# Performance work log

Measured on AMD Instinct MI355X. Metric: run time of the kernel, lower is better.

Reference implementation:

```python
import jax, jax.numpy as jnp
import numpy as np

N_NODES = 98304
N_GRAPHS = 2048
NODES_PER_GRAPH = 48
N_EDGES = 393216
NODE_IN = 128
EMB = 64
HID = 256
N_LAYERS = 6
ATTN_DIM = 256
N_HEADS = 4
HEAD_DIM = ATTN_DIM // N_HEADS
OUT_DIM = 1024


def setup_inputs() -> dict:
    key = jax.random.key(0)
    ks = iter(jax.random.split(key, 40))

    def nrm(shape, fan_in):
        return (jax.random.normal(next(ks), shape, dtype=jnp.float32)
                / np.float32(np.sqrt(fan_in)))

    x = jax.random.normal(next(ks), (N_NODES, NODE_IN), dtype=jnp.float32)
    edge_index = jax.random.randint(next(ks), (2, N_EDGES), 0, N_NODES, dtype=jnp.int32)
    batch = (jnp.arange(N_NODES, dtype=jnp.int32) // NODES_PER_GRAPH)

    inp = {
        "x": x,
        "edge_index": edge_index,
        "batch": batch,
        "W_embed": nrm((NODE_IN, EMB), NODE_IN),
        "b_embed": jnp.zeros((EMB,), jnp.float32),
        "W1": nrm((N_LAYERS, EMB, HID), EMB),
        "b1": jnp.zeros((N_LAYERS, HID), jnp.float32),
        "W2": nrm((N_LAYERS, HID, 2 * HID), HID),
        "b2": jnp.zeros((N_LAYERS, 2 * HID), jnp.float32),
        "W3": nrm((N_LAYERS, 2 * HID, EMB), 2 * HID),
        "b3": jnp.zeros((N_LAYERS, EMB), jnp.float32),
        "Wp": nrm((EMB, ATTN_DIM), EMB),
        "bp": jnp.zeros((ATTN_DIM,), jnp.float32),
        "q": jax.random.normal(next(ks), (1, ATTN_DIM), dtype=jnp.float32),
        "W_in": nrm((ATTN_DIM, 3 * ATTN_DIM), ATTN_DIM),
        "b_in": jnp.zeros((3 * ATTN_DIM,), jnp.float32),
        "W_out": nrm((ATTN_DIM, ATTN_DIM), ATTN_DIM),
        "b_out": jnp.zeros((ATTN_DIM,), jnp.float32),
        "Wh1": nrm((ATTN_DIM, HID), ATTN_DIM),
        "bh1": jnp.zeros((HID,), jnp.float32),
        "ln_g": jnp.ones((HID,), jnp.float32),
        "ln_b": jnp.zeros((HID,), jnp.float32),
        "Wh2": nrm((HID, OUT_DIM), HID),
        "bh2": jnp.zeros((OUT_DIM,), jnp.float32),
    }
    return inp


def _forward(x, edge_index, batch, W_embed, b_embed, W1, b1, W2, b2, W3, b3,
             Wp, bp, q, W_in, b_in, W_out, b_out, Wh1, bh1, ln_g, ln_b, Wh2, bh2):
    row = edge_index[0]  # only row is used, matching the torch module

    # node embed
    h = x @ W_embed + b_embed  # [N, 64]

    # 6 GNN layers: gather h[row] -> 3-layer MLP -> scatter_add back to row
    for l in range(N_LAYERS):
        m = jax.nn.relu(h[row] @ W1[l] + b1[l])          # [E, 256]
        m = jax.nn.relu(m @ W2[l] + b2[l])               # [E, 512]
        dh = m @ W3[l] + b3[l]                           # [E, 64]
        h = h + jax.ops.segment_sum(dh, row, num_segments=N_NODES)

    # attention pooling per graph (single learned query, 4 heads)
    hp = h @ Wp + bp                                     # [N, 256]
    Wq, Wk, Wv = W_in[:, :ATTN_DIM], W_in[:, ATTN_DIM:2 * ATTN_DIM], W_in[:, 2 * ATTN_DIM:]
    bq, bk, bv = b_in[:ATTN_DIM], b_in[ATTN_DIM:2 * ATTN_DIM], b_in[2 * ATTN_DIM:]

    qh = ((q @ Wq + bq).reshape(N_HEADS, HEAD_DIM)
          / jnp.asarray(np.sqrt(HEAD_DIM), jnp.float32))  # [H, D]
    k = (hp @ Wk + bk).reshape(N_NODES, N_HEADS, HEAD_DIM)
    v = (hp @ Wv + bv).reshape(N_NODES, N_HEADS, HEAD_DIM)

    scores = jnp.einsum('nhd,hd->nh', k, qh)             # [N, H]
    smax = jax.ops.segment_max(scores, batch, num_segments=N_GRAPHS)  # [B, H]
    e = jnp.exp(scores - smax[batch])
    denom = jax.ops.segment_sum(e, batch, num_segments=N_GRAPHS)      # [B, H]
    w = e / denom[batch]                                  # [N, H]
    pooled = jax.ops.segment_sum(w[:, :, None] * v, batch, num_segments=N_GRAPHS)  # [B, H, D]
    attn = pooled.reshape(N_GRAPHS, ATTN_DIM) @ W_out + b_out  # [B, 256]

    # projection head: ReLU -> Linear -> ReLU -> LayerNorm -> Linear
    t = jax.nn.relu(attn) @ Wh1 + bh1
    t = jax.nn.relu(t)
    mu = jnp.mean(t, axis=-1, keepdims=True)
    var = jnp.mean((t - mu) ** 2, axis=-1, keepdims=True)
    t = (t - mu) * jax.lax.rsqrt(var + 1e-5) * ln_g + ln_b
    return t @ Wh2 + bh2                                  # [B, 1024]


def reference(x, edge_index, batch, W_embed, b_embed, W1, b1, W2, b2, W3, b3,
              Wp, bp, q, W_in, b_in, W_out, b_out, Wh1, bh1, ln_g, ln_b, Wh2, bh2):
    return _forward(x, edge_index, batch, W_embed, b_embed, W1, b1, W2, b2, W3, b3,
                    Wp, bp, q, W_in, b_in, W_out, b_out, Wh1, bh1, ln_g, ln_b, Wh2, bh2)
```

## Files before the change

kernel.cpp:

```cpp
#include <hip/hip_runtime.h>
#include <hip/hip_bf16.h>

#define N_NODES 98304
#define N_GRAPHS 2048
#define N_EDGES 393216
#define EMB 64
#define HID 256
#define N_LAYERS_ 6

typedef __attribute__((ext_vector_type(8))) short short8v;
typedef __attribute__((ext_vector_type(4))) float f32x4;
#define MFMA16(a, b, c) __builtin_amdgcn_mfma_f32_16x16x32_bf16(a, b, c, 0, 0, 0)

__device__ __forceinline__ unsigned short f2bf(float x) {
    unsigned int u = __float_as_uint(x);
    u = (u + 0x7fffu + ((u >> 16) & 1u)) >> 16;
    return (unsigned short)u;
}
__device__ __forceinline__ float bf2f(unsigned short h) {
    return __uint_as_float(((unsigned int)h) << 16);
}
__device__ __forceinline__ unsigned int cvtpk(float a, float b) {
    unsigned int r;
    asm("v_cvt_pk_bf16_f32 %0, %1, %2" : "=v"(r) : "v"(a), "v"(b));
    return r;
}
__device__ __forceinline__ int swz(int row, int col, int rowc) {
    return (row * rowc + col) ^ ((row & 7) << 3);
}

__global__ __launch_bounds__(256) void zero_cnt_kernel(int* __restrict__ cnt) {
    int i = blockIdx.x * 256 + threadIdx.x;
    if (i < N_NODES) cnt[i] = 0;
}
__global__ __launch_bounds__(256) void hist_kernel(const int* __restrict__ row,
                                                   int* __restrict__ cnt) {
    int i = blockIdx.x * 256 + threadIdx.x;
    if (i < N_EDGES) atomicAdd(&cnt[row[i]], 1);
}

__global__ __launch_bounds__(64) void prep_frag_kernel(
    const float* __restrict__ W, unsigned short* __restrict__ oh,
    unsigned short* __restrict__ ol, int K, int N)
{
    const int NF = N >> 4, KS = K >> 5;
    const int fpl = NF * KS;
    const int layer = blockIdx.x / fpl;
    const int fid = blockIdx.x % fpl;
    const int nf = fid / KS, ks = fid % KS;
    const int lane = threadIdx.x;
    const float* Wl = W + (size_t)layer * K * N;
    const int n = nf * 16 + (lane & 15);
    const int kb = ks * 32 + (lane >> 4) * 8;
    short8v vh, vl;
    #pragma unroll
    for (int j = 0; j < 8; j++) {
        float wv = Wl[(size_t)(kb + j) * N + n];
        unsigned short hi = f2bf(wv);
        vh[j] = (short)hi;
        vl[j] = (short)f2bf(wv - bf2f(hi));
    }
    size_t o = (size_t)layer * K * N + ((size_t)(nf * KS + ks) * 64 + lane) * 8;
    *reinterpret_cast<short8v*>(oh + o) = vh;
    *reinterpret_cast<short8v*>(ol + o) = vl;
}

__global__ __launch_bounds__(256) void gbuild_kernel(
    const float* __restrict__ Wp, const float* __restrict__ bp,
    const float* __restrict__ W_in, const float* __restrict__ b_in,
    float* __restrict__ Gm, float* __restrict__ Gd)
{
    const int idx = blockIdx.x * 256 + threadIdx.x;
    const int q = idx >> 8, p = idx & 255;
    float s = 0.f;
    if ((q >> 6) == (p >> 6)) {
        const float* wr = Wp + (q & 63) * 256;
        for (int j = 0; j < 256; j++) s += wr[j] * W_in[j * 768 + 512 + p];
    }
    Gm[q * 256 + p] = s;
    if (blockIdx.x == 0) {
        const int pp = threadIdx.x;
        float dsum = b_in[512 + pp];
        for (int j = 0; j < 256; j++) dsum += bp[j] * W_in[j * 768 + 512 + pp];
        Gd[pp] = dsum;
    }
}

__global__ __launch_bounds__(256) void embed_mfma_kernel(
    const float* __restrict__ x,
    const unsigned short* __restrict__ Weh, const unsigned short* __restrict__ Wel,
    const float* __restrict__ b, float* __restrict__ h)
{
    __shared__ __attribute__((aligned(16))) unsigned short xh[32 * 128];
    __shared__ __attribute__((aligned(16))) unsigned short xl[32 * 128];
    const int tid = threadIdx.x;
    const int lane = tid & 63, w = tid >> 6;
    const int lm = lane & 15, lq = lane >> 4;
    const int base = blockIdx.x * 32;
    {
        int row = tid >> 3, c0 = (tid & 7) * 16;
        const float4* p = reinterpret_cast<const float4*>(x + (size_t)(base + row) * 128 + c0);
        #pragma unroll
        for (int g = 0; g < 4; g++) {
            float4 u = p[g];
            unsigned int p01 = cvtpk(u.x, u.y);
            unsigned int p23 = cvtpk(u.z, u.w);
            float h0 = __uint_as_float(p01 << 16), h1 = __uint_as_float(p01 & 0xffff0000u);
            float h2 = __uint_as_float(p23 << 16), h3 = __uint_as_float(p23 & 0xffff0000u);
            unsigned int q01 = cvtpk(u.x - h0, u.y - h1);
            unsigned int q23 = cvtpk(u.z - h2, u.w - h3);
            int idx = swz(row, c0 + g * 4, 128);
            *reinterpret_cast<uint2*>(&xh[idx]) = make_uint2(p01, p23);
            *reinterpret_cast<uint2*>(&xl[idx]) = make_uint2(q01, q23);
        }
    }
    __syncthreads();
    f32x4 acc0, acc1;
    {
        float bv = b[w * 16 + lm];
        acc0 = f32x4{bv, bv, bv, bv};
        acc1 = acc0;
    }
    #pragma unroll
    for (int ks = 0; ks < 4; ks++) {
        short8v a0h = *reinterpret_cast<const short8v*>(&xh[swz(lm, ks * 32 + lq * 8, 128)]);
        short8v a0l = *reinterpret_cast<const short8v*>(&xl[swz(lm, ks * 32 + lq * 8, 128)]);
        short8v a1h = *reinterpret_cast<const short8v*>(&xh[swz(16 + lm, ks * 32 + lq * 8, 128)]);
        short8v a1l = *reinterpret_cast<const short8v*>(&xl[swz(16 + lm, ks * 32 + lq * 8, 128)]);
        size_t bi = ((size_t)(w * 4 + ks) * 64 + lane) * 8;
        short8v bh = *reinterpret_cast<const short8v*>(Weh + bi);
        short8v bl = *reinterpret_cast<const short8v*>(Wel + bi);
        acc0 = MFMA16(a0h, bh, acc0); acc0 = MFMA16(a0l, bh, acc0); acc0 = MFMA16(a0h, bl, acc0);
        acc1 = MFMA16(a1h, bh, acc1); acc1 = MFMA16(a1l, bh, acc1); acc1 = MFMA16(a1h, bl, acc1);
    }
    #pragma unroll
    for (int r = 0; r < 4; r++) {
        h[(size_t)(base + lq * 4 + r) * 64 + w * 16 + lm] = acc0[r];
        h[(size_t)(base + 16 + lq * 4 + r) * 64 + w * 16 + lm] = acc1[r];
    }
}

__device__ __forceinline__ void store_quad(
    unsigned short* __restrict__ oh, unsigned short* __restrict__ ol,
    float v0, float v1, float v2, float v3,
    int row0, int col, int rowc)
{
    unsigned int p01 = cvtpk(v0, v1);
    unsigned int p23 = cvtpk(v2, v3);
    float h0 = __uint_as_float(p01 << 16), h1 = __uint_as_float(p01 & 0xffff0000u);
    float h2 = __uint_as_float(p23 << 16), h3 = __uint_as_float(p23 & 0xffff0000u);
    unsigned int q01 = cvtpk(v0 - h0, v1 - h1);
    unsigned int q23 = cvtpk(v2 - h2, v3 - h3);
    oh[swz(row0 + 0, col, rowc)] = (unsigned short)p01;
    oh[swz(row0 + 1, col, rowc)] = (unsigned short)(p01 >> 16);
    oh[swz(row0 + 2, col, rowc)] = (unsigned short)p23;
    oh[swz(row0 + 3, col, rowc)] = (unsigned short)(p23 >> 16);
    ol[swz(row0 + 0, col, rowc)] = (unsigned short)q01;
    ol[swz(row0 + 1, col, rowc)] = (unsigned short)(q01 >> 16);
    ol[swz(row0 + 2, col, rowc)] = (unsigned short)q23;
    ol[swz(row0 + 3, col, rowc)] = (unsigned short)(q23 >> 16);
}

__global__ __launch_bounds__(512, 6) void layer_mfma_kernel(
    float* __restrict__ h, const int* __restrict__ cnt,
    const unsigned short* __restrict__ W1h, const unsigned short* __restrict__ W1l,
    const float* __restrict__ b1,
    const unsigned short* __restrict__ W2h, const unsigned short* __restrict__ W2l,
    const float* __restrict__ b2,
    const unsigned short* __restrict__ W3h, const unsigned short* __restrict__ W3l,
    const float* __restrict__ b3)
{
    __shared__ __attribute__((aligned(16))) unsigned short R0[4096];
    __shared__ __attribute__((aligned(16))) unsigned short m1h_[8192];
    __shared__ __attribute__((aligned(16))) unsigned short m1l_[8192];
    __shared__ __attribute__((aligned(16))) unsigned short m2l_[4096];
    unsigned short* hsh = R0;
    unsigned short* hsl = R0 + 2048;
    unsigned short* m2h_ = R0;
    const int tid = threadIdx.x;
    const int lane = tid & 63, w = tid >> 6;
    const int lm = lane & 15, lq = lane >> 4;
    const int base = blockIdx.x * 32;

    {
        int row = tid >> 4, c0 = (tid & 15) * 4;
        const float4 u = *reinterpret_cast<const float4*>(h + (size_t)(base + row) * 64 + c0);
        unsigned int p01 = cvtpk(u.x, u.y);
        unsigned int p23 = cvtpk(u.z, u.w);
        float h0 = __uint_as_float(p01 << 16), h1 = __uint_as_float(p01 & 0xffff0000u);
        float h2 = __uint_as_float(p23 << 16), h3 = __uint_as_float(p23 & 0xffff0000u);
        unsigned int q01 = cvtpk(u.x - h0, u.y - h1);
        unsigned int q23 = cvtpk(u.z - h2, u.w - h3);
        int idx = swz(row, c0, 64);
        *reinterpret_cast<uint2*>(&hsh[idx]) = make_uint2(p01, p23);
        *reinterpret_cast<uint2*>(&hsl[idx]) = make_uint2(q01, q23);
    }
    __syncthreads();

    {
        f32x4 acc[2][2];
        #pragma unroll
        for (int f = 0; f < 2; f++) {
            float bv = b1[(2 * w + f) * 16 + lm];
            acc[f][0] = f32x4{bv, bv, bv, bv};
            acc[f][1] = acc[f][0];
        }
        #pragma unroll
        for (int ks = 0; ks < 2; ks++) {
            short8v ah0 = *reinterpret_cast<const short8v*>(&hsh[swz(lm, ks * 32 + lq * 8, 64)]);
            short8v al0 = *reinterpret_cast<const short8v*>(&hsl[swz(lm, ks * 32 + lq * 8, 64)]);
            short8v ah1 = *reinterpret_cast<const short8v*>(&hsh[swz(16 + lm, ks * 32 + lq * 8, 64)]);
            short8v al1 = *reinterpret_cast<const short8v*>(&hsl[swz(16 + lm, ks * 32 + lq * 8, 64)]);
            #pragma unroll
            for (int f = 0; f < 2; f++) {
                size_t bi = ((size_t)((2 * w + f) * 2 + ks) * 64 + lane) * 8;
                short8v bh = *reinterpret_cast<const short8v*>(W1h + bi);
                short8v bl = *reinterpret_cast<const short8v*>(W1l + bi);
                acc[f][0] = MFMA16(ah0, bh, acc[f][0]);
                acc[f][0] = MFMA16(al0, bh, acc[f][0]);
                acc[f][0] = MFMA16(ah0, bl, acc[f][0]);
                acc[f][1] = MFMA16(ah1, bh, acc[f][1]);
                acc[f][1] = MFMA16(al1, bh, acc[f][1]);
                acc[f][1] = MFMA16(ah1, bl, acc[f][1]);
            }
        }
        #pragma unroll
        for (int f = 0; f < 2; f++)
            #pragma unroll
            for (int m = 0; m < 2; m++)
                store_quad(m1h_, m1l_,
                           fmaxf(acc[f][m][0], 0.f), fmaxf(acc[f][m][1], 0.f),
                           fmaxf(acc[f][m][2], 0.f), fmaxf(acc[f][m][3], 0.f),
                           m * 16 + lq * 4, (2 * w + f) * 16 + lm, 256);
    }
    __syncthreads();

    const int nfc = w & 3, kq = w >> 2;
    f32x4 dacc[2];
    if (kq == 0) {
        float bv = b3[nfc * 16 + lm];
        dacc[0] = f32x4{bv, bv, bv, bv};
    } else {
        dacc[0] = f32x4{0.f, 0.f, 0.f, 0.f};
    }
    dacc[1] = dacc[0];

    #pragma unroll
    for (int c = 0; c < 4; ++c) {
        {
            const int nfg = c * 8 + w;
            f32x4 acc[2];
            {
                float bv = b2[nfg * 16 + lm];
                acc[0] = f32x4{bv, bv, bv, bv};
                acc[1] = acc[0];
            }
            #pragma unroll
            for (int ks = 0; ks < 8; ks++) {
                short8v ah0 = *reinterpret_cast<const short8v*>(&m1h_[swz(lm, ks * 32 + lq * 8, 256)]);
                short8v al0 = *reinterpret_cast<const short8v*>(&m1l_[swz(lm, ks * 32 + lq * 8, 256)]);
                short8v ah1 = *reinterpret_cast<const short8v*>(&m1h_[swz(16 + lm, ks * 32 + lq * 8, 256)]);
                short8v al1 = *reinterpret_cast<const short8v*>(&m1l_[swz(16 + lm, ks * 32 + lq * 8, 256)]);
                size_t bi = ((size_t)(nfg * 8 + ks) * 64 + lane) * 8;
                short8v bh = *reinterpret_cast<const short8v*>(W2h + bi);
                short8v bl = *reinterpret_cast<const short8v*>(W2l + bi);
                acc[0] = MFMA16(ah0, bh, acc[0]);
                acc[0] = MFMA16(al0, bh, acc[0]);
                acc[0] = MFMA16(ah0, bl, acc[0]);
                acc[1] = MFMA16(ah1, bh, acc[1]);
                acc[1] = MFMA16(al1, bh, acc[1]);
                acc[1] = MFMA16(ah1, bl, acc[1]);
            }
            #pragma unroll
            for (int m = 0; m < 2; m++)
                store_quad(m2h_, m2l_,
                           fmaxf(acc[m][0], 0.f), fmaxf(acc[m][1], 0.f),
                           fmaxf(acc[m][2], 0.f), fmaxf(acc[m][3], 0.f),
                           m * 16 + lq * 4, w * 16 + lm, 128);
        }
        __syncthreads();
        {
            #pragma unroll
            for (int kl = 0; kl < 2; kl++) {
                int ksl = kq * 2 + kl;
                short8v ah0 = *reinterpret_cast<const short8v*>(&m2h_[swz(lm, ksl * 32 + lq * 8, 128)]);
                short8v al0 = *reinterpret_cast<const short8v*>(&m2l_[swz(lm, ksl * 32 + lq * 8, 128)]);
                short8v ah1 = *reinterpret_cast<const short8v*>(&m2h_[swz(16 + lm, ksl * 32 + lq * 8, 128)]);
                short8v al1 = *reinterpret_cast<const short8v*>(&m2l_[swz(16 + lm, ksl * 32 + lq * 8, 128)]);
                int ksg = c * 4 + ksl;
                size_t bi = ((size_t)(nfc * 16 + ksg) * 64 + lane) * 8;
                short8v bh = *reinterpret_cast<const short8v*>(W3h + bi);
                short8v bl = *reinterpret_cast<const short8v*>(W3l + bi);
                dacc[0] = MFMA16(ah0, bh, dacc[0]);
                dacc[0] = MFMA16(al0, bh, dacc[0]);
                dacc[0] = MFMA16(ah0, bl, dacc[0]);
                dacc[1] = MFMA16(ah1, bh, dacc[1]);
                dacc[1] = MFMA16(al1, bh, dacc[1]);
                dacc[1] = MFMA16(ah1, bl, dacc[1]);
            }
        }
        __syncthreads();
    }

    float* scr = reinterpret_cast<float*>(m1h_);
    if (kq == 1) {
        #pragma unroll
        for (int m = 0; m < 2; m++)
            #pragma unroll
            for (int r = 0; r < 4; r++)
                scr[(m * 16 + lq * 4 + r) * 64 + nfc * 16 + lm] = dacc[m][r];
    }
    __syncthreads();
    if (kq == 0) {
        #pragma unroll
        for (int m = 0; m < 2; m++)
            #pragma unroll
            for (int r = 0; r < 4; r++) {
                int rr = base + m * 16 + lq * 4 + r;
                float dv = dacc[m][r] + scr[(m * 16 + lq * 4 + r) * 64 + nfc * 16 + lm];
                size_t gi = (size_t)rr * 64 + nfc * 16 + lm;
                h[gi] = h[gi] + (float)cnt[rr] * dv;
            }
    }
}

__global__ __launch_bounds__(256) void prec_kernel(
    const float* __restrict__ q, const float* __restrict__ W_in,
    const float* __restrict__ b_in, const float* __restrict__ Wp,
    const float* __restrict__ bp, float* __restrict__ prec)
{
    __shared__ float qh_s[256];
    __shared__ float u_s[4 * 256];
    const int tid = threadIdx.x;
    {
        float acc = b_in[tid];
        for (int j = 0; j < 256; j++) acc += q[j] * W_in[j * 768 + tid];
        qh_s[tid] = acc * 0.125f;
    }
    __syncthreads();
    {
        #pragma unroll
        for (int hd = 0; hd < 4; hd++) {
            float a = 0.f;
            for (int d = 0; d < 64; d++)
                a += W_in[tid * 768 + 256 + hd * 64 + d] * qh_s[hd * 64 + d];
            u_s[hd * 256 + tid] = a;
        }
    }
    __syncthreads();
    {
        int hd = tid >> 6, i = tid & 63;
        float a = 0.f;
        for (int j = 0; j < 256; j++) a += Wp[i * 256 + j] * u_s[hd * 256 + j];
        prec[hd * 64 + i] = a;
    }
    if (tid < 4) {
        float a = 0.f;
        for (int j = 0; j < 256; j++) a += bp[j] * u_s[tid * 256 + j];
        for (int d = 0; d < 64; d++) a += b_in[256 + tid * 64 + d] * qh_s[tid * 64 + d];
        prec[256 + tid] = a;
    }
}

__global__ __launch_bounds__(64) void attnpool_kernel(
    const float* __restrict__ h, const float* __restrict__ prec,
    float* __restrict__ hw)
{
    __shared__ float hs[48 * 65];
    __shared__ float ss[4 * 64];
    __shared__ float ds_[4];
    __shared__ float wl[48 * 4];
    const int lane = threadIdx.x;
    const int g = blockIdx.x;
    #pragma unroll
    for (int hd = 0; hd < 4; hd++) ss[hd * 64 + lane] = prec[hd * 64 + lane];
    if (lane < 4) ds_[lane] = prec[256 + lane];
    for (int r = 0; r < 48; r++)
        hs[r * 65 + lane] = h[((size_t)g * 48 + r) * 64 + lane];
    __syncthreads();
    float sc[4] = {0.f, 0.f, 0.f, 0.f};
    if (lane < 48) {
        #pragma unroll
        for (int hd = 0; hd < 4; hd++) sc[hd] = ds_[hd];
        for (int c = 0; c < 64; c++) {
            float a = hs[lane * 65 + c];
            #pragma unroll
            for (int hd = 0; hd < 4; hd++) sc[hd] += a * ss[hd * 64 + c];
        }
    }
    #pragma unroll
    for (int hd = 0; hd < 4; hd++) {
        float v = (lane < 48) ? sc[hd] : -3.0e38f;
        #pragma unroll
        for (int m = 32; m >= 1; m >>= 1) v = fmaxf(v, __shfl_xor(v, m, 64));
        float e = (lane < 48) ? __expf(sc[hd] - v) : 0.f;
        float s = e;
        #pragma unroll
        for (int m = 32; m >= 1; m >>= 1) s += __shfl_xor(s, m, 64);
        if (lane < 48) wl[lane * 4 + hd] = e / s;
    }
    __syncthreads();
    float acc[4] = {0.f, 0.f, 0.f, 0.f};
    for (int n = 0; n < 48; n++) {
        float hv = hs[n * 65 + lane];
        #pragma unroll
        for (int hd = 0; hd < 4; hd++) acc[hd] += wl[n * 4 + hd] * hv;
    }
    #pragma unroll
    for (int hd = 0; hd < 4; hd++) hw[(size_t)g * 256 + hd * 64 + lane] = acc[hd];
}

__device__ __forceinline__ void tail_stage(
    const unsigned short* __restrict__ inh, const unsigned short* __restrict__ inl,
    const unsigned short* __restrict__ wh, const unsigned short* __restrict__ wl,
    const float* __restrict__ bias, const bool do_relu,
    unsigned short* __restrict__ oth, unsigned short* __restrict__ otl,
    float* __restrict__ tf32,
    const int w, const int lane, const int lm, const int lq)
{
    f32x4 acc[2][2];
    #pragma unroll
    for (int f = 0; f < 2; f++) {
        float bv = bias[(2 * w + f) * 16 + lm];
        acc[f][0] = f32x4{bv, bv, bv, bv};
        acc[f][1] = acc[f][0];
    }
    #pragma unroll
    for (int ks = 0; ks < 8; ks++) {
        short8v ah0 = *reinterpret_cast<const short8v*>(&inh[swz(lm, ks * 32 + lq * 8, 256)]);
        short8v al0 = *reinterpret_cast<const short8v*>(&inl[swz(lm, ks * 32 + lq * 8, 256)]);
        short8v ah1 = *reinterpret_cast<const short8v*>(&inh[swz(16 + lm, ks * 32 + lq * 8, 256)]);
        short8v al1 = *reinterpret_cast<const short8v*>(&inl[swz(16 + lm, ks * 32 + lq * 8, 256)]);
        #pragma unroll
        for (int f = 0; f < 2; f++) {
            size_t bi = ((size_t)((2 * w + f) * 8 + ks) * 64 + lane) * 8;
            short8v bh = *reinterpret_cast<const short8v*>(wh + bi);
            short8v bl = *reinterpret_cast<const short8v*>(wl + bi);
            acc[f][0] = MFMA16(ah0, bh, acc[f][0]);
            acc[f][0] = MFMA16(al0, bh, acc[f][0]);
            acc[f][0] = MFMA16(ah0, bl, acc[f][0]);
            acc[f][1] = MFMA16(ah1, bh, acc[f][1]);
            acc[f][1] = MFMA16(al1, bh, acc[f][1]);
            acc[f][1] = MFMA16(ah1, bl, acc[f][1]);
        }
    }
    #pragma unroll
    for (int f = 0; f < 2; f++)
        #pragma unroll
        for (int m = 0; m < 2; m++) {
            if (tf32) {
                #pragma unroll
                for (int r = 0; r < 4; r++) {
                    float v = acc[f][m][r];
                    if (do_relu) v = fmaxf(v, 0.f);
                    tf32[(m * 16 + lq * 4 + r) * 256 + (2 * w + f) * 16 + lm] = v;
                }
            } else {
                float v0 = acc[f][m][0], v1 = acc[f][m][1], v2 = acc[f][m][2], v3 = acc[f][m][3];
                if (do_relu) {
                    v0 = fmaxf(v0, 0.f); v1 = fmaxf(v1, 0.f);
                    v2 = fmaxf(v2, 0.f); v3 = fmaxf(v3, 0.f);
                }
                store_quad(oth, otl, v0, v1, v2, v3,
                           m * 16 + lq * 4, (2 * w + f) * 16 + lm, 256);
            }
        }
}

__global__ __launch_bounds__(512, 4) void tail_mfma_kernel(
    const float* __restrict__ hw,
    const unsigned short* __restrict__ Gh, const unsigned short* __restrict__ Gl,
    const float* __restrict__ Gd,
    const unsigned short* __restrict__ Woh, const unsigned short* __restrict__ Wol,
    const float* __restrict__ b_out,
    const unsigned short* __restrict__ Wh1h, const unsigned short* __restrict__ Wh1l,
    const float* __restrict__ bh1,
    const float* __restrict__ ln_g, const float* __restrict__ ln_b,
    const unsigned short* __restrict__ Wh2h, const unsigned short* __restrict__ Wh2l,
    const float* __restrict__ bh2,
    float* __restrict__ out)
{
    __shared__ __attribute__((aligned(16))) unsigned short L[32768];
    unsigned short* Ah = L;
    unsigned short* Al = L + 8192;
    unsigned short* Bh = L + 16384;
    unsigned short* Bl = L + 24576;
    float* tf = reinterpret_cast<float*>(L + 16384);
    const int tid = threadIdx.x;
    const int lane = tid & 63, w = tid >> 6;
    const int lm = lane & 15, lq = lane >> 4;
    const int g0 = blockIdx.x * 32;

    {
        const float4* hp = reinterpret_cast<const float4*>(hw + (size_t)g0 * 256);
        #pragma unroll
        for (int i = 0; i < 4; i++) {
            int e = tid + 512 * i;
            int row = e >> 6, c0 = (e & 63) * 4;
            float4 u = hp[e];
            unsigned int p01 = cvtpk(u.x, u.y);
            unsigned int p23 = cvtpk(u.z, u.w);
            float h0 = __uint_as_float(p01 << 16), h1 = __uint_as_float(p01 & 0xffff0000u);
            float h2 = __uint_as_float(p23 << 16), h3 = __uint_as_float(p23 & 0xffff0000u);
            unsigned int q01 = cvtpk(u.x - h0, u.y - h1);
            unsigned int q23 = cvtpk(u.z - h2, u.w - h3);
            int idx = swz(row, c0, 256);
            *reinterpret_cast<uint2*>(&Ah[idx]) = make_uint2(p01, p23);
            *reinterpret_cast<uint2*>(&Al[idx]) = make_uint2(q01, q23);
        }
    }
    __syncthreads();
    tail_stage(Ah, Al, Gh, Gl, Gd, false, Bh, Bl, nullptr, w, lane, lm, lq);
    __syncthreads();
    tail_stage(Bh, Bl, Woh, Wol, b_out, true, Ah, Al, nullptr, w, lane, lm, lq);
    __syncthreads();
    tail_stage(Ah, Al, Wh1h, Wh1l, bh1, true, nullptr, nullptr, tf, w, lane, lm, lq);
    __syncthreads();
    {
        const int row = tid >> 4, l16 = tid & 15;
        float s = 0.f;
        #pragma unroll
        for (int k = 0; k < 16; k++) s += tf[row * 256 + l16 + 16 * k];
        #pragma unroll
        for (int m = 1; m < 16; m <<= 1) s += __shfl_xor(s, m, 16);
        float mu = s * (1.f / 256.f);
        float v = 0.f;
        #pragma unroll
        for (int k = 0; k < 16; k++) {
            float d = tf[row * 256 + l16 + 16 * k] - mu;
            v += d * d;
        }
        #pragma unroll
        for (int m = 1; m < 16; m <<= 1) v += __shfl_xor(v, m, 16);
        float rs = rsqrtf(v * (1.f / 256.f) + 1e-5f);
        #pragma unroll
        for (int k = 0; k < 16; k++) {
            int col = l16 + 16 * k;
            float val = (tf[row * 256 + col] - mu) * rs * ln_g[col] + ln_b[col];
            unsigned short hi = f2bf(val);
            int idx = swz(row, col, 256);
            Ah[idx] = hi;
            Al[idx] = f2bf(val - bf2f(hi));
        }
    }
    __syncthreads();
    {
        f32x4 acc[8][2];
        #pragma unroll
        for (int f = 0; f < 8; f++) {
            float bv = bh2[(8 * w + f) * 16 + lm];
            acc[f][0] = f32x4{bv, bv, bv, bv};
            acc[f][1] = acc[f][0];
        }
        #pragma unroll
        for (int ks = 0; ks < 8; ks++) {
            short8v ah0 = *reinterpret_cast<const short8v*>(&Ah[swz(lm, ks * 32 + lq * 8, 256)]);
            short8v al0 = *reinterpret_cast<const short8v*>(&Al[swz(lm, ks * 32 + lq * 8, 256)]);
            short8v ah1 = *reinterpret_cast<const short8v*>(&Ah[swz(16 + lm, ks * 32 + lq * 8, 256)]);
            short8v al1 = *reinterpret_cast<const short8v*>(&Al[swz(16 + lm, ks * 32 + lq * 8, 256)]);
            #pragma unroll
            for (int f = 0; f < 8; f++) {
                size_t bi = ((size_t)((8 * w + f) * 8 + ks) * 64 + lane) * 8;
                short8v bh = *reinterpret_cast<const short8v*>(Wh2h + bi);
                short8v bl = *reinterpret_cast<const short8v*>(Wh2l + bi);
                acc[f][0] = MFMA16(ah0, bh, acc[f][0]);
                acc[f][0] = MFMA16(al0, bh, acc[f][0]);
                acc[f][0] = MFMA16(ah0, bl, acc[f][0]);
                acc[f][1] = MFMA16(ah1, bh, acc[f][1]);
                acc[f][1] = MFMA16(al1, bh, acc[f][1]);
                acc[f][1] = MFMA16(ah1, bl, acc[f][1]);
            }
        }
        #pragma unroll
        for (int f = 0; f < 8; f++)
            #pragma unroll
            for (int m = 0; m < 2; m++)
                #pragma unroll
                for (int r = 0; r < 4; r++)
                    out[(size_t)(g0 + m * 16 + lq * 4 + r) * 1024 + (8 * w + f) * 16 + lm]
                        = acc[f][m][r];
    }
}

extern "C" void kernel_launch(void* const* d_in, const int* in_sizes, int n_in,
                              void* d_out, int out_size, void* d_ws, size_t ws_size,
                              hipStream_t stream) {
    const float* x       = (const float*)d_in[0];
    const int*   edge    = (const int*)d_in[1];
    const float* W_embed = (const float*)d_in[3];
    const float* b_embed = (const float*)d_in[4];
    const float* W1 = (const float*)d_in[5];
    const float* b1 = (const float*)d_in[6];
    const float* W2 = (const float*)d_in[7];
    const float* b2 = (const float*)d_in[8];
    const float* W3 = (const float*)d_in[9];
    const float* b3 = (const float*)d_in[10];
    const float* Wp = (const float*)d_in[11];
    const float* bp = (const float*)d_in[12];
    const float* q  = (const float*)d_in[13];
    const float* W_in  = (const float*)d_in[14];
    const float* b_in  = (const float*)d_in[15];
    const float* W_out = (const float*)d_in[16];
    const float* b_out = (const float*)d_in[17];
    const float* Wh1 = (const float*)d_in[18];
    const float* bh1 = (const float*)d_in[19];
    const float* ln_g = (const float*)d_in[20];
    const float* ln_b = (const float*)d_in[21];
    const float* Wh2 = (const float*)d_in[22];
    const float* bh2 = (const float*)d_in[23];
    float* out = (float*)d_out;

    char* ws = (char*)d_ws;
    int*   cnt  = (int*)(ws + 0);
    float* h    = (float*)(ws + 393216);
    float* hw   = (float*)(ws + 25559040);
    float* prec = (float*)(ws + 27656192);
    unsigned short* W1h = (unsigned short*)(ws + 27657232);
    unsigned short* W1l = (unsigned short*)(ws + 27853840);
    unsigned short* W2h = (unsigned short*)(ws + 28050448);
    unsigned short* W2l = (unsigned short*)(ws + 29623312);
    unsigned short* W3h = (unsigned short*)(ws + 31196176);
    unsigned short* W3l = (unsigned short*)(ws + 31589392);
    unsigned short* Weh = (unsigned short*)(ws + 31982608);
    unsigned short* Wel = (unsigned short*)(ws + 31998992);
    float* Gm  = (float*)(ws + 32015376);
    float* Gd  = (float*)(ws + 32277520);
    unsigned short* Gfh  = (unsigned short*)(ws + 32278544);
    unsigned short* Gfl  = (unsigned short*)(ws + 32409616);
    unsigned short* Wofh = (unsigned short*)(ws + 32540688);
    unsigned short* Wofl = (unsigned short*)(ws + 32671760);
    unsigned short* Wh1fh= (unsigned short*)(ws + 32802832);
    unsigned short* Wh1fl= (unsigned short*)(ws + 32933904);
    unsigned short* Wh2fh= (unsigned short*)(ws + 33064976);
    unsigned short* Wh2fl= (unsigned short*)(ws + 33589264);

    zero_cnt_kernel<<<N_NODES / 256, 256, 0, stream>>>(cnt);
    hist_kernel<<<N_EDGES / 256, 256, 0, stream>>>(edge, cnt);

    prep_frag_kernel<<<1 * (64 / 16) * (128 / 32), 64, 0, stream>>>(W_embed, Weh, Wel, 128, 64);
    prep_frag_kernel<<<6 * (256 / 16) * (64 / 32), 64, 0, stream>>>(W1, W1h, W1l, 64, 256);
    prep_frag_kernel<<<6 * (512 / 16) * (256 / 32), 64, 0, stream>>>(W2, W2h, W2l, 256, 512);
    prep_frag_kernel<<<6 * (64 / 16) * (512 / 32), 64, 0, stream>>>(W3, W3h, W3l, 512, 64);

    gbuild_kernel<<<256, 256, 0, stream>>>(Wp, bp, W_in, b_in, Gm, Gd);
    prep_frag_kernel<<<(256 / 16) * (256 / 32), 64, 0, stream>>>(Gm, Gfh, Gfl, 256, 256);
    prep_frag_kernel<<<(256 / 16) * (256 / 32), 64, 0, stream>>>(W_out, Wofh, Wofl, 256, 256);
    prep_frag_kernel<<<(256 / 16) * (256 / 32), 64, 0, stream>>>(Wh1, Wh1fh, Wh1fl, 256, 256);
    prep_frag_kernel<<<(1024 / 16) * (256 / 32), 64, 0, stream>>>(Wh2, Wh2fh, Wh2fl, 256, 1024);

    embed_mfma_kernel<<<N_NODES / 32, 256, 0, stream>>>(x, Weh, Wel, b_embed, h);
    for (int l = 0; l < N_LAYERS_; l++) {
        layer_mfma_kernel<<<N_NODES / 32, 512, 0, stream>>>(
            h, cnt,
            W1h + (size_t)l * EMB * HID,     W1l + (size_t)l * EMB * HID,     b1 + (size_t)l * HID,
            W2h + (size_t)l * HID * 2 * HID, W2l + (size_t)l * HID * 2 * HID, b2 + (size_t)l * 2 * HID,
            W3h + (size_t)l * 2 * HID * EMB, W3l + (size_t)l * 2 * HID * EMB, b3 + (size_t)l * EMB);
    }
    prec_kernel<<<1, 256, 0, stream>>>(q, W_in, b_in, Wp, bp, prec);
    attnpool_kernel<<<N_GRAPHS, 64, 0, stream>>>(h, prec, hw);
    tail_mfma_kernel<<<N_GRAPHS / 32, 512, 0, stream>>>(
        hw, Gfh, Gfl, Gd, Wofh, Wofl, b_out, Wh1fh, Wh1fl, bh1,
        ln_g, ln_b, Wh2fh, Wh2fl, bh2, out);
}
```

Measured before the change: 877.5 us.

## Switch GNN layer kernel to 32x32x16 MFMA with wider chunks and new LDS plan

Rewrites the per-layer MLP kernel to use 32x32x16 bf16 MFMA tiles instead of 16x16x32. Weights are pre-fragmented in the matching 32-wide layout, W2 is processed in two 256-column chunks instead of four 128-column chunks, and the final reduction goes through a 4-way LDS scratch with a vectorised float4 update of h. The goal is fewer B-fragment loads per MFMA and fewer barriers and chunk iterations. In exchange, LDS grows to 64 KB per block, occupancy is lowered to 4 waves per SIMD, and an extra barrier is added inside each chunk.

```diff
diff --git a/kernel.cpp b/kernel.cpp
--- a/kernel.cpp
+++ b/kernel.cpp
@@ -10,7 +10,9 @@
 
 typedef __attribute__((ext_vector_type(8))) short short8v;
 typedef __attribute__((ext_vector_type(4))) float f32x4;
+typedef __attribute__((ext_vector_type(16))) float f32x16;
 #define MFMA16(a, b, c) __builtin_amdgcn_mfma_f32_16x16x32_bf16(a, b, c, 0, 0, 0)
+#define MFMA32(a, b, c) __builtin_amdgcn_mfma_f32_32x32x16_bf16(a, b, c, 0, 0, 0)
 
 __device__ __forceinline__ unsigned short f2bf(float x) {
     unsigned int u = __float_as_uint(x);
@@ -26,7 +28,7 @@
     return r;
 }
 __device__ __forceinline__ int swz(int row, int col, int rowc) {
-    return (row * rowc + col) ^ ((row & 7) << 3);
+    return (row * rowc + col) ^ ((row & ((rowc >> 3) - 1)) << 3);
 }
 
 __global__ __launch_bounds__(256) void zero_cnt_kernel(int* __restrict__ cnt) {
@@ -52,6 +54,32 @@
     const float* Wl = W + (size_t)layer * K * N;
     const int n = nf * 16 + (lane & 15);
     const int kb = ks * 32 + (lane >> 4) * 8;
+    short8v vh, vl;
+    #pragma unroll
+    for (int j = 0; j < 8; j++) {
+        float wv = Wl[(size_t)(kb + j) * N + n];
+        unsigned short hi = f2bf(wv);
+        vh[j] = (short)hi;
+        vl[j] = (short)f2bf(wv - bf2f(hi));
+    }
+    size_t o = (size_t)layer * K * N + ((size_t)(nf * KS + ks) * 64 + lane) * 8;
+    *reinterpret_cast<short8v*>(oh + o) = vh;
+    *reinterpret_cast<short8v*>(ol + o) = vl;
+}
+
+__global__ __launch_bounds__(64) void prep_frag32_kernel(
+    const float* __restrict__ W, unsigned short* __restrict__ oh,
+    unsigned short* __restrict__ ol, int K, int N)
+{
+    const int NF = N >> 5, KS = K >> 4;
+    const int fpl = NF * KS;
+    const int layer = blockIdx.x / fpl;
+    const int fid = blockIdx.x % fpl;
+    const int nf = fid / KS, ks = fid % KS;
+    const int lane = threadIdx.x;
+    const float* Wl = W + (size_t)layer * K * N;
+    const int n = nf * 32 + (lane & 31);
+    const int kb = ks * 16 + (lane >> 5) * 8;
     short8v vh, vl;
     #pragma unroll
     for (int j = 0; j < 8; j++) {
@@ -161,7 +189,7 @@
     ol[swz(row0 + 3, col, rowc)] = (unsigned short)(q23 >> 16);
 }
 
-__global__ __launch_bounds__(512, 6) void layer_mfma_kernel(
+__global__ __launch_bounds__(512, 4) void layer_mfma_kernel(
     float* __restrict__ h, const int* __restrict__ cnt,
     const unsigned short* __restrict__ W1h, const unsigned short* __restrict__ W1l,
     const float* __restrict__ b1,
@@ -170,16 +198,19 @@
     const unsigned short* __restrict__ W3h, const unsigned short* __restrict__ W3l,
     const float* __restrict__ b3)
 {
-    __shared__ __attribute__((aligned(16))) unsigned short R0[4096];
-    __shared__ __attribute__((aligned(16))) unsigned short m1h_[8192];
-    __shared__ __attribute__((aligned(16))) unsigned short m1l_[8192];
-    __shared__ __attribute__((aligned(16))) unsigned short m2l_[4096];
-    unsigned short* hsh = R0;
-    unsigned short* hsl = R0 + 2048;
-    unsigned short* m2h_ = R0;
+    __shared__ __attribute__((aligned(16))) unsigned short m1_[16384];
+    __shared__ __attribute__((aligned(16))) unsigned short m2_[16384];
+    unsigned short* m1h_ = m1_;
+    unsigned short* m1l_ = m1_ + 8192;
+    unsigned short* m2h_ = m2_;
+    unsigned short* m2l_ = m2_ + 8192;
+    unsigned short* hsh = m2_;
+    unsigned short* hsl = m2_ + 2048;
+    float* scr = reinterpret_cast<float*>(m1_);
+
     const int tid = threadIdx.x;
     const int lane = tid & 63, w = tid >> 6;
-    const int lm = lane & 15, lq = lane >> 4;
+    const int lr = lane & 31, lh = lane >> 5;
     const int base = blockIdx.x * 32;
 
     {
@@ -198,129 +229,118 @@
     __syncthreads();
 
     {
-        f32x4 acc[2][2];
-        #pragma unroll
-        for (int f = 0; f < 2; f++) {
-            float bv = b1[(2 * w + f) * 16 + lm];
-            acc[f][0] = f32x4{bv, bv, bv, bv};
-            acc[f][1] = acc[f][0];
-        }
-        #pragma unroll
-        for (int ks = 0; ks < 2; ks++) {
-            short8v ah0 = *reinterpret_cast<const short8v*>(&hsh[swz(lm, ks * 32 + lq * 8, 64)]);
-            short8v al0 = *reinterpret_cast<const short8v*>(&hsl[swz(lm, ks * 32 + lq * 8, 64)]);
-            short8v ah1 = *reinterpret_cast<const short8v*>(&hsh[swz(16 + lm, ks * 32 + lq * 8, 64)]);
-            short8v al1 = *reinterpret_cast<const short8v*>(&hsl[swz(16 + lm, ks * 32 + lq * 8, 64)]);
+        f32x16 a0, a1;
+        float bv = b1[w * 32 + lr];
+        #pragma unroll
+        for (int i = 0; i < 16; i++) { a0[i] = bv; a1[i] = 0.f; }
+        #pragma unroll
+        for (int ks = 0; ks < 4; ks++) {
+            short8v ah = *reinterpret_cast<const short8v*>(&hsh[swz(lr, ks * 16 + lh * 8, 64)]);
+            short8v al = *reinterpret_cast<const short8v*>(&hsl[swz(lr, ks * 16 + lh * 8, 64)]);
+            size_t bi = ((size_t)(w * 4 + ks) * 64 + lane) * 8;
+            short8v bh = *reinterpret_cast<const short8v*>(W1h + bi);
+            short8v bl = *reinterpret_cast<const short8v*>(W1l + bi);
+            if (ks & 1) {
+                a1 = MFMA32(ah, bh, a1); a1 = MFMA32(al, bh, a1); a1 = MFMA32(ah, bl, a1);
+            } else {
+                a0 = MFMA32(ah, bh, a0); a0 = MFMA32(al, bh, a0); a0 = MFMA32(ah, bl, a0);
+            }
+        }
+        #pragma unroll
+        for (int q = 0; q < 4; q++)
+            store_quad(m1h_, m1l_,
+                fmaxf(a0[4 * q + 0] + a1[4 * q + 0], 0.f),
+                fmaxf(a0[4 * q + 1] + a1[4 * q + 1], 0.f),
+                fmaxf(a0[4 * q + 2] + a1[4 * q + 2], 0.f),
+                fmaxf(a0[4 * q + 3] + a1[4 * q + 3], 0.f),
+                8 * q + 4 * lh, w * 32 + lr, 256);
+    }
+    __syncthreads();
+
+    const int nfc = w & 1, kq = w >> 1;
+    f32x16 d0, d1;
+    {
+        float bv = (kq == 0) ? b3[nfc * 32 + lr] : 0.f;
+        #pragma unroll
+        for (int i = 0; i < 16; i++) { d0[i] = bv; d1[i] = 0.f; }
+    }
+
+    #pragma unroll
+    for (int c = 0; c < 2; ++c) {
+        {
+            const int nf = c * 8 + w;
+            f32x16 a0, a1;
+            float bv = b2[nf * 32 + lr];
             #pragma unroll
-            for (int f = 0; f < 2; f++) {
-                size_t bi = ((size_t)((2 * w + f) * 2 + ks) * 64 + lane) * 8;
-                short8v bh = *reinterpret_cast<const short8v*>(W1h + bi);
-                short8v bl = *reinterpret_cast<const short8v*>(W1l + bi);
-                acc[f][0] = MFMA16(ah0, bh, acc[f][0]);
-                acc[f][0] = MFMA16(al0, bh, acc[f][0]);
-                acc[f][0] = MFMA16(ah0, bl, acc[f][0]);
-                acc[f][1] = MFMA16(ah1, bh, acc[f][1]);
-                acc[f][1] = MFMA16(al1, bh, acc[f][1]);
-                acc[f][1] = MFMA16(ah1, bl, acc[f][1]);
-            }
-        }
-        #pragma unroll
-        for (int f = 0; f < 2; f++)
+            for (int i = 0; i < 16; i++) { a0[i] = bv; a1[i] = 0.f; }
             #pragma unroll
-            for (int m = 0; m < 2; m++)
-                store_quad(m1h_, m1l_,
-                           fmaxf(acc[f][m][0], 0.f), fmaxf(acc[f][m][1], 0.f),
-                           fmaxf(acc[f][m][2], 0.f), fmaxf(acc[f][m][3], 0.f),
-                           m * 16 + lq * 4, (2 * w + f) * 16 + lm, 256);
-    }
-    __syncthreads();
-
-    const int nfc = w & 3, kq = w >> 2;
-    f32x4 dacc[2];
-    if (kq == 0) {
-        float bv = b3[nfc * 16 + lm];
-        dacc[0] = f32x4{bv, bv, bv, bv};
-    } else {
-        dacc[0] = f32x4{0.f, 0.f, 0.f, 0.f};
-    }
-    dacc[1] = dacc[0];
-
-    #pragma unroll
-    for (int c = 0; c < 4; ++c) {
-        {
-            const int nfg = c * 8 + w;
-            f32x4 acc[2];
-            {
-                float bv = b2[nfg * 16 + lm];
-                acc[0] = f32x4{bv, bv, bv, bv};
-                acc[1] = acc[0];
-            }
-            #pragma unroll
-            for (int ks = 0; ks < 8; ks++) {
-                short8v ah0 = *reinterpret_cast<const short8v*>(&m1h_[swz(lm, ks * 32 + lq * 8, 256)]);
-                short8v al0 = *reinterpret_cast<const short8v*>(&m1l_[swz(lm, ks * 32 + lq * 8, 256)]);
-                short8v ah1 = *reinterpret_cast<const short8v*>(&m1h_[swz(16 + lm, ks * 32 + lq * 8, 256)]);
-                short8v al1 = *reinterpret_cast<const short8v*>(&m1l_[swz(16 + lm, ks * 32 + lq * 8, 256)]);
-                size_t bi = ((size_t)(nfg * 8 + ks) * 64 + lane) * 8;
+            for (int kk = 0; kk < 16; kk++) {
+                short8v ah = *reinterpret_cast<const short8v*>(&m1h_[swz(lr, kk * 16 + lh * 8, 256)]);
+                short8v al = *reinterpret_cast<const short8v*>(&m1l_[swz(lr, kk * 16 + lh * 8, 256)]);
+                size_t bi = ((size_t)(nf * 16 + kk) * 64 + lane) * 8;
                 short8v bh = *reinterpret_cast<const short8v*>(W2h + bi);
                 short8v bl = *reinterpret_cast<const short8v*>(W2l + bi);
-                acc[0] = MFMA16(ah0, bh, acc[0]);
-                acc[0] = MFMA16(al0, bh, acc[0]);
-                acc[0] = MFMA16(ah0, bl, acc[0]);
-                acc[1] = MFMA16(ah1, bh, acc[1]);
-                acc[1] = MFMA16(al1, bh, acc[1]);
-                acc[1] = MFMA16(ah1, bl, acc[1]);
+                if (kk & 1) {
+                    a1 = MFMA32(ah, bh, a1); a1 = MFMA32(al, bh, a1); a1 = MFMA32(ah, bl, a1);
+                } else {
+                    a0 = MFMA32(ah, bh, a0); a0 = MFMA32(al, bh, a0); a0 = MFMA32(ah, bl, a0);
+                }
             }
+            __syncthreads();
             #pragma unroll
-            for (int m = 0; m < 2; m++)
+            for (int q = 0; q < 4; q++)
                 store_quad(m2h_, m2l_,
-                           fmaxf(acc[m][0], 0.f), fmaxf(acc[m][1], 0.f),
-                           fmaxf(acc[m][2], 0.f), fmaxf(acc[m][3], 0.f),
-                           m * 16 + lq * 4, w * 16 + lm, 128);
+                    fmaxf(a0[4 * q + 0] + a1[4 * q + 0], 0.f),
+                    fmaxf(a0[4 * q + 1] + a1[4 * q + 1], 0.f),
+                    fmaxf(a0[4 * q + 2] + a1[4 * q + 2], 0.f),
+                    fmaxf(a0[4 * q + 3] + a1[4 * q + 3], 0.f),
+                    8 * q + 4 * lh, w * 32 + lr, 256);
         }
         __syncthreads();
-        {
-            #pragma unroll
-            for (int kl = 0; kl < 2; kl++) {
-                int ksl = kq * 2 + kl;
-                short8v ah0 = *reinterpret_cast<const short8v*>(&m2h_[swz(lm, ksl * 32 + lq * 8, 128)]);
-                short8v al0 = *reinterpret_cast<const short8v*>(&m2l_[swz(lm, ksl * 32 + lq * 8, 128)]);
-                short8v ah1 = *reinterpret_cast<const short8v*>(&m2h_[swz(16 + lm, ksl * 32 + lq * 8, 128)]);
-                short8v al1 = *reinterpret_cast<const short8v*>(&m2l_[swz(16 + lm, ksl * 32 + lq * 8, 128)]);
-                int ksg = c * 4 + ksl;
-                size_t bi = ((size_t)(nfc * 16 + ksg) * 64 + lane) * 8;
-                short8v bh = *reinterpret_cast<const short8v*>(W3h + bi);
-                short8v bl = *reinterpret_cast<const short8v*>(W3l + bi);
-                dacc[0] = MFMA16(ah0, bh, dacc[0]);
-                dacc[0] = MFMA16(al0, bh, dacc[0]);
-                dacc[0] = MFMA16(ah0, bl, dacc[0]);
-                dacc[1] = MFMA16(ah1, bh, dacc[1]);
-                dacc[1] = MFMA16(al1, bh, dacc[1]);
-                dacc[1] = MFMA16(ah1, bl, dacc[1]);
+        #pragma unroll
+        for (int kk = 0; kk < 4; kk++) {
+            int kg = kq * 4 + kk;
+            short8v ah = *reinterpret_cast<const short8v*>(&m2h_[swz(lr, kg * 16 + lh * 8, 256)]);
+            short8v al = *reinterpret_cast<const short8v*>(&m2l_[swz(lr, kg * 16 + lh * 8, 256)]);
+            size_t bi = ((size_t)(nfc * 32 + c * 16 + kg) * 64 + lane) * 8;
+            short8v bh = *reinterpret_cast<const short8v*>(W3h + bi);
+            short8v bl = *reinterpret_cast<const short8v*>(W3l + bi);
+            if (kk & 1) {
+                d1 = MFMA32(ah, bh, d1); d1 = MFMA32(al, bh, d1); d1 = MFMA32(ah, bl, d1);
+            } else {
+                d0 = MFMA32(ah, bh, d0); d0 = MFMA32(al, bh, d0); d0 = MFMA32(ah, bl, d0);
             }
         }
-        __syncthreads();
-    }
-
-    float* scr = reinterpret_cast<float*>(m1h_);
-    if (kq == 1) {
-        #pragma unroll
-        for (int m = 0; m < 2; m++)
-            #pragma unroll
-            for (int r = 0; r < 4; r++)
-                scr[(m * 16 + lq * 4 + r) * 64 + nfc * 16 + lm] = dacc[m][r];
-    }
-    __syncthreads();
-    if (kq == 0) {
-        #pragma unroll
-        for (int m = 0; m < 2; m++)
+    }
+    __syncthreads();
+
+    {
+        f32x16 dv = d0 + d1;
+        #pragma unroll
+        for (int q = 0; q < 4; q++)
             #pragma unroll
             for (int r = 0; r < 4; r++) {
-                int rr = base + m * 16 + lq * 4 + r;
-                float dv = dacc[m][r] + scr[(m * 16 + lq * 4 + r) * 64 + nfc * 16 + lm];
-                size_t gi = (size_t)rr * 64 + nfc * 16 + lm;
-                h[gi] = h[gi] + (float)cnt[rr] * dv;
+                int row = 8 * q + 4 * lh + r;
+                scr[kq * 2048 + row * 64 + nfc * 32 + lr] = dv[4 * q + r];
             }
+    }
+    __syncthreads();
+    {
+        int i0 = tid * 4;
+        int row = i0 >> 6, col = i0 & 63;
+        int rr = base + row;
+        float cv = (float)cnt[rr];
+        f32x4 s0 = *reinterpret_cast<f32x4*>(&scr[i0]);
+        f32x4 s1 = *reinterpret_cast<f32x4*>(&scr[2048 + i0]);
+        f32x4 s2 = *reinterpret_cast<f32x4*>(&scr[4096 + i0]);
+        f32x4 s3 = *reinterpret_cast<f32x4*>(&scr[6144 + i0]);
+        float4* hp = reinterpret_cast<float4*>(h + (size_t)rr * 64 + col);
+        float4 hv = *hp;
+        hv.x += cv * (s0[0] + s1[0] + s2[0] + s3[0]);
+        hv.y += cv * (s0[1] + s1[1] + s2[1] + s3[1]);
+        hv.z += cv * (s0[2] + s1[2] + s2[2] + s3[2]);
+        hv.w += cv * (s0[3] + s1[3] + s2[3] + s3[3]);
+        *hp = hv;
     }
 }
 
@@ -638,9 +658,9 @@
     hist_kernel<<<N_EDGES / 256, 256, 0, stream>>>(edge, cnt);
 
     prep_frag_kernel<<<1 * (64 / 16) * (128 / 32), 64, 0, stream>>>(W_embed, Weh, Wel, 128, 64);
-    prep_frag_kernel<<<6 * (256 / 16) * (64 / 32), 64, 0, stream>>>(W1, W1h, W1l, 64, 256);
-    prep_frag_kernel<<<6 * (512 / 16) * (256 / 32), 64, 0, stream>>>(W2, W2h, W2l, 256, 512);
-    prep_frag_kernel<<<6 * (64 / 16) * (512 / 32), 64, 0, stream>>>(W3, W3h, W3l, 512, 64);
+    prep_frag32_kernel<<<6 * (256 / 32) * (64 / 16), 64, 0, stream>>>(W1, W1h, W1l, 64, 256);
+    prep_frag32_kernel<<<6 * (512 / 32) * (256 / 16), 64, 0, stream>>>(W2, W2h, W2l, 256, 512);
+    prep_frag32_kernel<<<6 * (64 / 32) * (512 / 16), 64, 0, stream>>>(W3, W3h, W3l, 512, 64);
 
     gbuild_kernel<<<256, 256, 0, stream>>>(Wp, bp, W_in, b_in, Gm, Gd);
     prep_frag_kernel<<<(256 / 16) * (256 / 32), 64, 0, stream>>>(Gm, Gfh, Gfl, 256, 256);
```

Result: slower. 895.8 us (+2.1%).

## Prefetch weight fragments into registers ahead of MFMA use in layer kernel

Applied to the files above, without the earlier changes.

Issues the W1 fragment loads before the h tile is converted to LDS, double-buffers the W2 fragment loads one k-pair ahead inside the MLP loop, and fetches W3 fragments before the barrier that precedes their use, so global-load latency overlaps with MFMA work. The swizzle mask now scales with row width instead of being fixed at 8 rows. The launch-bounds occupancy hint drops from 6 to 4 blocks per CU, giving the compiler more registers for the prefetched fragments at the cost of fewer resident waves to hide latency.

```diff
diff --git a/kernel.cpp b/kernel.cpp
--- a/kernel.cpp
+++ b/kernel.cpp
@@ -26,7 +26,7 @@
     return r;
 }
 __device__ __forceinline__ int swz(int row, int col, int rowc) {
-    return (row * rowc + col) ^ ((row & 7) << 3);
+    return (row * rowc + col) ^ ((row & ((rowc >> 3) - 1)) << 3);
 }
 
 __global__ __launch_bounds__(256) void zero_cnt_kernel(int* __restrict__ cnt) {
@@ -161,7 +161,7 @@
     ol[swz(row0 + 3, col, rowc)] = (unsigned short)(q23 >> 16);
 }
 
-__global__ __launch_bounds__(512, 6) void layer_mfma_kernel(
+__global__ __launch_bounds__(512, 4) void layer_mfma_kernel(
     float* __restrict__ h, const int* __restrict__ cnt,
     const unsigned short* __restrict__ W1h, const unsigned short* __restrict__ W1l,
     const float* __restrict__ b1,
@@ -182,16 +182,26 @@
     const int lm = lane & 15, lq = lane >> 4;
     const int base = blockIdx.x * 32;
 
-    {
-        int row = tid >> 4, c0 = (tid & 15) * 4;
-        const float4 u = *reinterpret_cast<const float4*>(h + (size_t)(base + row) * 64 + c0);
-        unsigned int p01 = cvtpk(u.x, u.y);
-        unsigned int p23 = cvtpk(u.z, u.w);
+    int s0row = tid >> 4, s0c = (tid & 15) * 4;
+    const float4 u0 = *reinterpret_cast<const float4*>(h + (size_t)(base + s0row) * 64 + s0c);
+
+    const unsigned short* pAh = W1h + ((size_t)(4 * w) * 64 + lane) * 8;
+    const unsigned short* pAl = W1l + ((size_t)(4 * w) * 64 + lane) * 8;
+    short8v awh[4], awl[4];
+    #pragma unroll
+    for (int i = 0; i < 4; i++) {
+        awh[i] = *reinterpret_cast<const short8v*>(pAh + (size_t)i * 512);
+        awl[i] = *reinterpret_cast<const short8v*>(pAl + (size_t)i * 512);
+    }
+
+    {
+        unsigned int p01 = cvtpk(u0.x, u0.y);
+        unsigned int p23 = cvtpk(u0.z, u0.w);
         float h0 = __uint_as_float(p01 << 16), h1 = __uint_as_float(p01 & 0xffff0000u);
         float h2 = __uint_as_float(p23 << 16), h3 = __uint_as_float(p23 & 0xffff0000u);
-        unsigned int q01 = cvtpk(u.x - h0, u.y - h1);
-        unsigned int q23 = cvtpk(u.z - h2, u.w - h3);
-        int idx = swz(row, c0, 64);
+        unsigned int q01 = cvtpk(u0.x - h0, u0.y - h1);
+        unsigned int q23 = cvtpk(u0.z - h2, u0.w - h3);
+        int idx = swz(s0row, s0c, 64);
         *reinterpret_cast<uint2*>(&hsh[idx]) = make_uint2(p01, p23);
         *reinterpret_cast<uint2*>(&hsl[idx]) = make_uint2(q01, q23);
     }
@@ -213,9 +223,8 @@
             short8v al1 = *reinterpret_cast<const short8v*>(&hsl[swz(16 + lm, ks * 32 + lq * 8, 64)]);
             #pragma unroll
             for (int f = 0; f < 2; f++) {
-                size_t bi = ((size_t)((2 * w + f) * 2 + ks) * 64 + lane) * 8;
-                short8v bh = *reinterpret_cast<const short8v*>(W1h + bi);
-                short8v bl = *reinterpret_cast<const short8v*>(W1l + bi);
+                short8v bh = awh[2 * f + ks];
+                short8v bl = awl[2 * f + ks];
                 acc[f][0] = MFMA16(ah0, bh, acc[f][0]);
                 acc[f][0] = MFMA16(al0, bh, acc[f][0]);
                 acc[f][0] = MFMA16(ah0, bl, acc[f][0]);
@@ -247,29 +256,62 @@
 
     #pragma unroll
     for (int c = 0; c < 4; ++c) {
+        short8v cwh[2], cwl[2];
         {
             const int nfg = c * 8 + w;
+            const unsigned short* pBh = W2h + ((size_t)(nfg * 8) * 64 + lane) * 8;
+            const unsigned short* pBl = W2l + ((size_t)(nfg * 8) * 64 + lane) * 8;
             f32x4 acc[2];
             {
                 float bv = b2[nfg * 16 + lm];
                 acc[0] = f32x4{bv, bv, bv, bv};
                 acc[1] = acc[0];
             }
-            #pragma unroll
-            for (int ks = 0; ks < 8; ks++) {
-                short8v ah0 = *reinterpret_cast<const short8v*>(&m1h_[swz(lm, ks * 32 + lq * 8, 256)]);
-                short8v al0 = *reinterpret_cast<const short8v*>(&m1l_[swz(lm, ks * 32 + lq * 8, 256)]);
-                short8v ah1 = *reinterpret_cast<const short8v*>(&m1h_[swz(16 + lm, ks * 32 + lq * 8, 256)]);
-                short8v al1 = *reinterpret_cast<const short8v*>(&m1l_[swz(16 + lm, ks * 32 + lq * 8, 256)]);
-                size_t bi = ((size_t)(nfg * 8 + ks) * 64 + lane) * 8;
-                short8v bh = *reinterpret_cast<const short8v*>(W2h + bi);
-                short8v bl = *reinterpret_cast<const short8v*>(W2l + bi);
-                acc[0] = MFMA16(ah0, bh, acc[0]);
-                acc[0] = MFMA16(al0, bh, acc[0]);
-                acc[0] = MFMA16(ah0, bl, acc[0]);
-                acc[1] = MFMA16(ah1, bh, acc[1]);
-                acc[1] = MFMA16(al1, bh, acc[1]);
-                acc[1] = MFMA16(ah1, bl, acc[1]);
+            short8v whE = *reinterpret_cast<const short8v*>(pBh);
+            short8v wlE = *reinterpret_cast<const short8v*>(pBl);
+            short8v whO = *reinterpret_cast<const short8v*>(pBh + 512);
+            short8v wlO = *reinterpret_cast<const short8v*>(pBl + 512);
+            #pragma unroll
+            for (int kp = 0; kp < 4; kp++) {
+                const int k0 = 2 * kp;
+                short8v whE2, wlE2, whO2, wlO2;
+                if (kp < 3) {
+                    whE2 = *reinterpret_cast<const short8v*>(pBh + (size_t)(k0 + 2) * 512);
+                    wlE2 = *reinterpret_cast<const short8v*>(pBl + (size_t)(k0 + 2) * 512);
+                    whO2 = *reinterpret_cast<const short8v*>(pBh + (size_t)(k0 + 3) * 512);
+                    wlO2 = *reinterpret_cast<const short8v*>(pBl + (size_t)(k0 + 3) * 512);
+                }
+                {
+                    short8v ah0 = *reinterpret_cast<const short8v*>(&m1h_[swz(lm, k0 * 32 + lq * 8, 256)]);
+                    short8v al0 = *reinterpret_cast<const short8v*>(&m1l_[swz(lm, k0 * 32 + lq * 8, 256)]);
+                    short8v ah1 = *reinterpret_cast<const short8v*>(&m1h_[swz(16 + lm, k0 * 32 + lq * 8, 256)]);
+                    short8v al1 = *reinterpret_cast<const short8v*>(&m1l_[swz(16 + lm, k0 * 32 + lq * 8, 256)]);
+                    acc[0] = MFMA16(ah0, whE, acc[0]);
+                    acc[0] = MFMA16(al0, whE, acc[0]);
+                    acc[0] = MFMA16(ah0, wlE, acc[0]);
+                    acc[1] = MFMA16(ah1, whE, acc[1]);
+                    acc[1] = MFMA16(al1, whE, acc[1]);
+                    acc[1] = MFMA16(ah1, wlE, acc[1]);
+                }
+                {
+                    short8v ah0 = *reinterpret_cast<const short8v*>(&m1h_[swz(lm, (k0 + 1) * 32 + lq * 8, 256)]);
+                    short8v al0 = *reinterpret_cast<const short8v*>(&m1l_[swz(lm, (k0 + 1) * 32 + lq * 8, 256)]);
+                    short8v ah1 = *reinterpret_cast<const short8v*>(&m1h_[swz(16 + lm, (k0 + 1) * 32 + lq * 8, 256)]);
+                    short8v al1 = *reinterpret_cast<const short8v*>(&m1l_[swz(16 + lm, (k0 + 1) * 32 + lq * 8, 256)]);
+                    acc[0] = MFMA16(ah0, whO, acc[0]);
+                    acc[0] = MFMA16(al0, whO, acc[0]);
+                    acc[0] = MFMA16(ah0, wlO, acc[0]);
+                    acc[1] = MFMA16(ah1, whO, acc[1]);
+                    acc[1] = MFMA16(al1, whO, acc[1]);
+                    acc[1] = MFMA16(ah1, wlO, acc[1]);
+                }
+                if (kp < 3) { whE = whE2; wlE = wlE2; whO = whO2; wlO = wlO2; }
+            }
+            #pragma unroll
+            for (int kl = 0; kl < 2; kl++) {
+                size_t bi = ((size_t)(nfc * 16 + c * 4 + kq * 2 + kl) * 64 + lane) * 8;
+                cwh[kl] = *reinterpret_cast<const short8v*>(W3h + bi);
+                cwl[kl] = *reinterpret_cast<const short8v*>(W3l + bi);
             }
             #pragma unroll
             for (int m = 0; m < 2; m++)
@@ -287,16 +329,12 @@
                 short8v al0 = *reinterpret_cast<const short8v*>(&m2l_[swz(lm, ksl * 32 + lq * 8, 128)]);
                 short8v ah1 = *reinterpret_cast<const short8v*>(&m2h_[swz(16 + lm, ksl * 32 + lq * 8, 128)]);
                 short8v al1 = *reinterpret_cast<const short8v*>(&m2l_[swz(16 + lm, ksl * 32 + lq * 8, 128)]);
-                int ksg = c * 4 + ksl;
-                size_t bi = ((size_t)(nfc * 16 + ksg) * 64 + lane) * 8;
-                short8v bh = *reinterpret_cast<const short8v*>(W3h + bi);
-                short8v bl = *reinterpret_cast<const short8v*>(W3l + bi);
-                dacc[0] = MFMA16(ah0, bh, dacc[0]);
-                dacc[0] = MFMA16(al0, bh, dacc[0]);
-                dacc[0] = MFMA16(ah0, bl, dacc[0]);
-                dacc[1] = MFMA16(ah1, bh, dacc[1]);
-                dacc[1] = MFMA16(al1, bh, dacc[1]);
-                dacc[1] = MFMA16(ah1, bl, dacc[1]);
+                dacc[0] = MFMA16(ah0, cwh[kl], dacc[0]);
+                dacc[0] = MFMA16(al0, cwh[kl], dacc[0]);
+                dacc[0] = MFMA16(ah0, cwl[kl], dacc[0]);
+                dacc[1] = MFMA16(ah1, cwh[kl], dacc[1]);
+                dacc[1] = MFMA16(al1, cwh[kl], dacc[1]);
+                dacc[1] = MFMA16(ah1, cwl[kl], dacc[1]);
             }
         }
         __syncthreads();
```

Measured after the change: 885.2 us. About the same (+0.9%).
